# Optimization experiments

Hardware: AMD Instinct MI355X
Metric: run time of the kernel (lower is better)

## Reference

```python
import jax, jax.numpy as jnp
import numpy as np

# Static configuration (mirrors MeshPotential.__init__ + mesh-size derivation)
SIGMA = 1.0          # atomic_gaussian_width
SPACING = 0.2        # mesh_spacing
ORDER = 4            # interpolation_order (cubic, P3M M4 assignment)
L = 10.0             # cubic cell edge used in setup_inputs
N_ATOMS = 200000
# ns = 2**ceil(log2(2*L/SPACING + 1)) = 2**ceil(log2(101)) = 128 per axis
NX = NY = NZ = 128


def setup_inputs() -> dict:
    key = jax.random.key(0)
    k1, k2 = jax.random.split(key)
    cell = L * jnp.eye(3, dtype=jnp.float32)                  # (3,3) cell rows = basis vectors
    positions = jax.random.uniform(k1, (N_ATOMS, 3), jnp.float32, 0.0, L)
    charges = jax.random.normal(k2, (N_ATOMS, 1), jnp.float32)
    return {"cell": cell, "positions": positions, "charges": charges}


def _interp(cell, positions):
    """Order-4 (cubic B-spline / P3M) interpolation weights + flat mesh indices."""
    ns = jnp.array([NX, NY, NZ], dtype=positions.dtype)
    rel = (positions @ jnp.linalg.inv(cell)) * ns             # (n,3) fractional * mesh size
    idx0 = jnp.floor(rel).astype(jnp.int32)                   # even order: floor-based stencil
    x = rel - (idx0.astype(rel.dtype) + 0.5)                  # offset in [-1/2, 1/2)
    x2, x3 = x * x, x * x * x
    # P3M charge-assignment weights of order 4, grid points [floor-1, floor, floor+1, floor+2]
    w = jnp.stack([
        1.0 - 6.0 * x + 12.0 * x2 - 8.0 * x3,
        23.0 - 30.0 * x - 12.0 * x2 + 24.0 * x3,
        23.0 + 30.0 * x - 12.0 * x2 - 24.0 * x3,
        1.0 + 6.0 * x + 12.0 * x2 + 8.0 * x3,
    ]) / 48.0                                                 # (4, n, 3)
    shifts = jnp.array([-1, 0, 1, 2], dtype=jnp.int32)
    idx = (idx0[None] + shifts[:, None, None]) % jnp.array([NX, NY, NZ], jnp.int32)  # (4,n,3)
    ix, iy, iz = idx[..., 0], idx[..., 1], idx[..., 2]        # (4,n) each
    flat = (ix[:, None, None] * NY + iy[None, :, None]) * NZ + iz[None, None, :]     # (4,4,4,n)
    flat = flat.reshape(64, -1).T                             # (n,64) flat mesh indices
    w3d = jnp.einsum('ia,ja,ka->aijk', w[..., 0], w[..., 1], w[..., 2]).reshape(-1, 64)  # (n,64)
    return w3d, flat


def _forward(cell, positions, charges):
    n, C = charges.shape
    w3d, flat = _interp(cell, positions)
    # points_to_mesh: spline-weighted scatter of charges onto the mesh
    vals = charges.T[:, :, None] * w3d[None]                  # (C,n,64)
    rho = jnp.zeros((C, NX * NY * NZ), charges.dtype).at[:, flat].add(vals)
    rho = rho.reshape(C, NX, NY, NZ)
    # Fourier-space convolution with G(k^2) = 4*pi/k^2 * exp(-sigma^2 k^2 / 2), G(0)=0
    Brec = 2.0 * jnp.pi * jnp.linalg.inv(cell).T              # rows = reciprocal vectors b_i
    mx = jnp.fft.fftfreq(NX) * NX
    my = jnp.fft.fftfreq(NY) * NY
    mz = jnp.fft.rfftfreq(NZ) * NZ
    kvec = (mx[:, None, None, None] * Brec[0]
            + my[None, :, None, None] * Brec[1]
            + mz[None, None, :, None] * Brec[2])              # (NX,NY,NZ//2+1,3)
    ksq = jnp.sum(kvec * kvec, axis=-1).astype(charges.dtype)
    safe = jnp.where(ksq == 0.0, 1.0, ksq)
    G = jnp.where(ksq == 0.0, 0.0, 4.0 * jnp.pi / safe * jnp.exp(-0.5 * SIGMA * SIGMA * safe))
    rho_hat = jnp.fft.rfftn(rho, axes=(1, 2, 3))              # unnormalized forward FFT
    pot_mesh = jnp.fft.irfftn(rho_hat * G, s=(NX, NY, NZ), axes=(1, 2, 3), norm="forward")
    pot_mesh = pot_mesh / jnp.abs(jnp.linalg.det(cell))       # divide by cell volume
    # mesh_to_points: spline-weighted gather back to atom positions
    gathered = pot_mesh.reshape(C, -1)[:, flat] * w3d[None]   # (C,n,64)
    potential = gathered.sum(-1).T                            # (n,C)
    # subtract self-contribution of the atom-centered gaussian
    potential = potential - charges * (jnp.sqrt(2.0 / jnp.pi) / SIGMA)
    return potential


def reference(cell, positions, charges):
    return _forward(cell, positions, charges)
```

## Files before the change

### kernel.cpp

```cpp
#include <hip/hip_runtime.h>
#include <math.h>

#define NTOT (128*128*128)
#define NBIN2 64
#define BINS (NBIN2*NBIN2*NBIN2)
#define SCAN_BLOCKS 256

#define ZP 72
#define CAP 1024

#define PI_F      3.14159265358979323846f
#define TWO_PI_F  6.28318530717958647692f
#define FOUR_PI_F 12.5663706143591729539f


__device__ inline void inv3x3(const float* __restrict__ c, float* inv, float* detOut) {
    float a = c[0], b = c[1], cc = c[2];
    float d = c[3], e = c[4], f  = c[5];
    float g = c[6], h = c[7], i  = c[8];
    float A = e * i - f * h;
    float B = f * g - d * i;
    float C = d * h - e * g;
    float det = a * A + b * B + cc * C;
    float r = 1.0f / det;
    inv[0] = A * r;              inv[1] = (cc * h - b * i) * r;  inv[2] = (b * f - cc * e) * r;
    inv[3] = B * r;              inv[4] = (a * i - cc * g) * r;  inv[5] = (cc * d - a * f) * r;
    inv[6] = C * r;              inv[7] = (b * g - a * h) * r;   inv[8] = (a * e - b * d) * r;
    *detOut = det;
}

__device__ inline void w4(float x, float* w) {
    float x2 = x * x, x3 = x2 * x;
    w[0] = (1.0f  - 6.0f  * x + 12.0f * x2 - 8.0f  * x3) * (1.0f / 48.0f);
    w[1] = (23.0f - 30.0f * x - 12.0f * x2 + 24.0f * x3) * (1.0f / 48.0f);
    w[2] = (23.0f + 30.0f * x - 12.0f * x2 - 24.0f * x3) * (1.0f / 48.0f);
    w[3] = (1.0f  + 6.0f  * x + 12.0f * x2 + 8.0f  * x3) * (1.0f / 48.0f);
}

__device__ inline void atom_rel(const float* __restrict__ cell,
                                const float* __restrict__ pos, int t,
                                float* rx, float* ry, float* rz) {
    float inv[9]; float det;
    inv3x3(cell, inv, &det);
    float px = pos[3 * t], py = pos[3 * t + 1], pz = pos[3 * t + 2];
    *rx = (px * inv[0] + py * inv[3] + pz * inv[6]) * 128.0f;
    *ry = (px * inv[1] + py * inv[4] + pz * inv[7]) * 128.0f;
    *rz = (px * inv[2] + py * inv[5] + pz * inv[8]) * 128.0f;
}

__device__ inline int bin_of(float rx, float ry, float rz) {
    int ix = ((int)floorf(rx)) & 127;
    int iy = ((int)floorf(ry)) & 127;
    int iz = ((int)floorf(rz)) & 127;
    return ((((ix >> 1) << 6) | (iy >> 1)) << 6) | (iz >> 1);
}

__device__ inline float wrap128(float u) {
    u = (u > 64.0f) ? u - 128.0f : u;
    u = (u < -64.0f) ? u + 128.0f : u;
    return u;
}

__device__ inline float bspline(float u) {
    float a = fabsf(u);
    float t = fmaxf(2.0f - a, 0.0f);
    float s = fmaxf(1.0f - a, 0.0f);
    return t * t * t - 4.0f * s * s * s;
}


__global__ void zero_int_kernel(int* __restrict__ p, int n) {
    int i = blockIdx.x * blockDim.x + threadIdx.x;
    if (i < n) p[i] = 0;
}

__global__ void hist_kernel(const float* __restrict__ cell, const float* __restrict__ pos,
                            int* __restrict__ hist, int n) {
    int t = blockIdx.x * blockDim.x + threadIdx.x;
    if (t >= n) return;
    float rx, ry, rz;
    atom_rel(cell, pos, t, &rx, &ry, &rz);
    atomicAdd(&hist[bin_of(rx, ry, rz)], 1);
}

__global__ __launch_bounds__(256) void scan_local(const int4* __restrict__ hist4,
                                                  int4* __restrict__ off4,
                                                  int* __restrict__ partials) {
    const int b = blockIdx.x, t = threadIdx.x;
    const int idx = b * 256 + t;
    int4 h = hist4[idx];
    int s = h.x + h.y + h.z + h.w;
    int lane = t & 63, wv = t >> 6;
    int v = s;
    #pragma unroll
    for (int d = 1; d < 64; d <<= 1) {
        int o = __shfl_up(v, d, 64);
        if (lane >= d) v += o;
    }
    __shared__ int wsum[4];
    if (lane == 63) wsum[wv] = v;
    __syncthreads();
    int add = 0;
    #pragma unroll
    for (int k = 0; k < 4; ++k) if (k < wv) add += wsum[k];
    int run = add + v - s;
    int4 o4;
    o4.x = run; run += h.x;
    o4.y = run; run += h.y;
    o4.z = run; run += h.z;
    o4.w = run; run += h.w;
    off4[idx] = o4;
    if (t == 255) partials[b] = run;
}

__global__ __launch_bounds__(256) void scan_add(int4* __restrict__ hist4,
                                                int4* __restrict__ off4,
                                                const int* __restrict__ partials,
                                                int* __restrict__ offsets) {
    const int b = blockIdx.x, t = threadIdx.x;
    int lane = t & 63, wv = t >> 6;
    int v = (t < b) ? partials[t] : 0;
    #pragma unroll
    for (int d = 32; d >= 1; d >>= 1) v += __shfl_xor(v, d, 64);
    __shared__ int ws2[4];
    __shared__ int base_s;
    if (lane == 0) ws2[wv] = v;
    __syncthreads();
    if (t == 0) base_s = ws2[0] + ws2[1] + ws2[2] + ws2[3];
    __syncthreads();
    const int base = base_s;
    const int idx = b * 256 + t;
    int4 o4 = off4[idx];
    o4.x += base; o4.y += base; o4.z += base; o4.w += base;
    off4[idx]  = o4;
    hist4[idx] = o4;
    if (b == SCAN_BLOCKS - 1 && t == 255) offsets[BINS] = base + partials[b];
}

__global__ void reorder_kernel(const float* __restrict__ cell, const float* __restrict__ pos,
                               const float* __restrict__ q, int* __restrict__ cursor,
                               float4* __restrict__ sorted, int* __restrict__ sortedIdx, int n) {
    int t = blockIdx.x * blockDim.x + threadIdx.x;
    if (t >= n) return;
    float rx, ry, rz;
    atom_rel(cell, pos, t, &rx, &ry, &rz);
    int p = atomicAdd(&cursor[bin_of(rx, ry, rz)], 1);
    sorted[p] = make_float4(rx, ry, rz, q[t]);
    sortedIdx[p] = t;
}


__global__ __launch_bounds__(512) void lds_scatter_kernel(const float4* __restrict__ atoms,
                                                          const int* __restrict__ offsets,
                                                          float* __restrict__ rmesh) {
    const int blk = blockIdx.x;
    const int bz = blk & 7, by = (blk >> 3) & 7, bx = blk >> 6;
    const int ox = bx << 4, oy = by << 4, oz = bz << 4;
    const int gbx0 = ((ox - 2) & 127) >> 1;
    const int gby0 = ((oy - 2) & 127) >> 1;
    const int gbz0 = ((oz - 2) & 127) >> 1;

    __shared__ float4 satoms[CAP];
    __shared__ int P[1025];
    __shared__ int wsum[8];

    const int t = threadIdx.x;

    int c0 = 0, c1 = 0, g0 = 0, g1 = 0;
    {
        int b = 2 * t;
        if (b < 1000) {
            int jx = b / 100, rr = b - jx * 100, jy = rr / 10, jz = rr - jy * 10;
            int gb = ((((gbx0 + jx) & 63) << 6) | ((gby0 + jy) & 63)) << 6 | ((gbz0 + jz) & 63);
            g0 = offsets[gb]; c0 = offsets[gb + 1] - g0;
        }
        b = 2 * t + 1;
        if (b < 1000) {
            int jx = b / 100, rr = b - jx * 100, jy = rr / 10, jz = rr - jy * 10;
            int gb = ((((gbx0 + jx) & 63) << 6) | ((gby0 + jy) & 63)) << 6 | ((gbz0 + jz) & 63);
            g1 = offsets[gb]; c1 = offsets[gb + 1] - g1;
        }
    }

    int s = c0 + c1;
    int lane = t & 63, wv = t >> 6;
    int v = s;
    #pragma unroll
    for (int d = 1; d < 64; d <<= 1) {
        int o = __shfl_up(v, d, 64);
        if (lane >= d) v += o;
    }
    if (lane == 63) wsum[wv] = v;
    __syncthreads();
    int add = 0;
    #pragma unroll
    for (int k = 0; k < 8; ++k) if (k < wv) add += wsum[k];
    const int pre = add + v - s;
    P[2 * t] = pre;
    P[2 * t + 1] = pre + c0;
    if (t == 511) P[1024] = add + v;
    __syncthreads();

    for (int k = 0; k < c0; ++k) {
        int d = pre + k;
        if (d >= CAP) break;
        satoms[d] = atoms[g0 + k];
    }
    {
        int pre1 = pre + c0;
        for (int k = 0; k < c1; ++k) {
            int d = pre1 + k;
            if (d >= CAP) break;
            satoms[d] = atoms[g1 + k];
        }
    }
    __syncthreads();

    const int qz = t & 7, qy = (t >> 3) & 7, qx = t >> 6;
    const int cx0 = ox + (qx << 1), cy0 = oy + (qy << 1), cz0 = oz + (qz << 1);
    const float fcx = (float)cx0, fcy = (float)cy0, fcz = (float)cz0;

    float a000 = 0.0f, a001 = 0.0f, a010 = 0.0f, a011 = 0.0f;
    float a100 = 0.0f, a101 = 0.0f, a110 = 0.0f, a111 = 0.0f;

    int r = -1, i = 0, e = 0;
    while (i >= e) {
        if (++r >= 9) break;
        int dbx = r / 3, dby = r - dbx * 3;
        int bin0 = ((qx + dbx) * 10 + (qy + dby)) * 10 + qz;
        i = P[bin0];
        e = P[bin0 + 3];
        if (e > CAP) e = CAP;
    }
    while (r < 9) {
        float4 a = satoms[i];

        float ux = wrap128(a.x - fcx);
        float wx0 = bspline(ux);
        float wx1 = bspline(ux - 1.0f);
        float uy = wrap128(a.y - fcy);
        float wy0 = bspline(uy);
        float wy1 = bspline(uy - 1.0f);
        float uz = wrap128(a.z - fcz);
        float wz0 = bspline(uz);
        float wz1 = bspline(uz - 1.0f);
        float qs = a.w * (1.0f / 216.0f);
        float qx0 = qs * wx0, qx1 = qs * wx1;
        float m00 = qx0 * wy0, m01 = qx0 * wy1;
        float m10 = qx1 * wy0, m11 = qx1 * wy1;
        a000 += m00 * wz0; a001 += m00 * wz1;
        a010 += m01 * wz0; a011 += m01 * wz1;
        a100 += m10 * wz0; a101 += m10 * wz1;
        a110 += m11 * wz0; a111 += m11 * wz1;

        if (++i >= e) {
            while (i >= e) {
                if (++r >= 9) break;
                int dbx = r / 3, dby = r - dbx * 3;
                int bin0 = ((qx + dbx) * 10 + (qy + dby)) * 10 + qz;
                i = P[bin0];
                e = P[bin0 + 3];
                if (e > CAP) e = CAP;
            }
            if (r >= 9) break;
        }
    }

    *(float2*)&rmesh[((size_t)cx0       << 14) | ((size_t)cy0       << 7) | (size_t)cz0] = make_float2(a000, a001);
    *(float2*)&rmesh[((size_t)cx0       << 14) | ((size_t)(cy0 + 1) << 7) | (size_t)cz0] = make_float2(a010, a011);
    *(float2*)&rmesh[((size_t)(cx0 + 1) << 14) | ((size_t)cy0       << 7) | (size_t)cz0] = make_float2(a100, a101);
    *(float2*)&rmesh[((size_t)(cx0 + 1) << 14) | ((size_t)(cy0 + 1) << 7) | (size_t)cz0] = make_float2(a110, a111);
}


__device__ inline void bfly_dif(float& rr, float& ii, int h, bool hi, float cs, float sn) {
    float pr = __shfl_xor(rr, h), pi = __shfl_xor(ii, h);
    float br = hi ? (pr - rr) : (rr + pr);
    float bi = hi ? (pi - ii) : (ii + pi);
    rr = cs * br - sn * bi;
    ii = cs * bi + sn * br;
}

__device__ inline void bfly_dit(float& rr, float& ii, int h, bool hi, float cs, float sn) {
    float pr = __shfl_xor(rr, h), pi = __shfl_xor(ii, h);
    float xr = hi ? rr : pr, xi = hi ? ii : pi;
    float br = hi ? pr : rr, bi = hi ? pi : ii;
    float tr = cs * xr - sn * xi, ti = cs * xi + sn * xr;
    rr = hi ? (br - tr) : (br + tr);
    ii = hi ? (bi - ti) : (bi + ti);
}

__device__ inline void wfft_dif_fwd(float& r0, float& i0, float& r1, float& i1, int lane) {
    {
        float ang = -PI_F * (float)lane * (1.0f / 64.0f);
        float sn, cs; __sincosf(ang, &sn, &cs);
        float ar = r0 + r1, ai = i0 + i1;
        float dr = r0 - r1, di = i0 - i1;
        r0 = ar; i0 = ai;
        r1 = cs * dr - sn * di;
        i1 = cs * di + sn * dr;
    }
    #pragma unroll
    for (int h = 32; h >= 1; h >>= 1) {
        int pos = lane & (h - 1);
        bool hi = (lane & h) != 0;
        float ang = hi ? (-PI_F * (float)pos / (float)h) : 0.0f;
        float sn, cs; __sincosf(ang, &sn, &cs);
        bfly_dif(r0, i0, h, hi, cs, sn);
        bfly_dif(r1, i1, h, hi, cs, sn);
    }
}

__device__ inline void wfft_dit_inv(float& r0, float& i0, float& r1, float& i1, int lane) {
    #pragma unroll
    for (int h = 1; h <= 32; h <<= 1) {
        int pos = lane & (h - 1);
        bool hi = (lane & h) != 0;
        float ang = PI_F * (float)pos / (float)h;
        float sn, cs; __sincosf(ang, &sn, &cs);
        bfly_dit(r0, i0, h, hi, cs, sn);
        bfly_dit(r1, i1, h, hi, cs, sn);
    }
    {
        float ang = PI_F * (float)lane * (1.0f / 64.0f);
        float sn, cs; __sincosf(ang, &sn, &cs);
        float tr = cs * r1 - sn * i1, ti = cs * i1 + sn * r1;
        float nr = r0 + tr, ni = i0 + ti;
        r1 = r0 - tr; i1 = i0 - ti;
        r0 = nr; i0 = ni;
    }
}


__global__ __launch_bounds__(1024) void fftZfwd(const float* __restrict__ rin,
                                                float2* __restrict__ mesh) {
    __shared__ float tre[16][132], tim[16][132];
    const int t = threadIdx.x, b = blockIdx.x;
    for (int u = t; u < 2048; u += 1024) {
        int l = u >> 7, e = u & 127;
        tre[l][e] = rin[((size_t)((b << 4) | l) << 7) + e];
    }
    __syncthreads();
    const int w = t >> 6, lane = t & 63;
    float r0 = tre[w][lane],      i0 = 0.0f;
    float r1 = tre[w][lane + 64], i1 = 0.0f;
    wfft_dif_fwd(r0, i0, r1, i1, lane);
    int e0 = (int)(__brev((unsigned)lane) >> 25);
    tre[w][e0] = r0;     tim[w][e0] = i0;
    tre[w][e0 + 1] = r1; tim[w][e0 + 1] = i1;
    __syncthreads();
    for (int u = t; u < 2048; u += 1024) {
        int l = u >> 7, e = u & 127;
        if (e < ZP)
            mesh[(size_t)((b << 4) | l) * ZP + e] = make_float2(tre[l][e], tim[l][e]);
    }
}


__global__ __launch_bounds__(512) void fftYfwd(float2* __restrict__ mesh) {
    __shared__ float tre[8][132], tim[8][132];
    const int t = threadIdx.x, b = blockIdx.x;
    const int x = b & 127, zf0 = (b >> 7) << 3;
    const size_t rb = ((size_t)(x << 7)) * ZP + zf0;
    for (int u = t; u < 1024; u += 512) {
        int e = u >> 3, dz = u & 7;
        float2 vv = mesh[rb + (size_t)e * ZP + dz];
        tre[dz][e] = vv.x; tim[dz][e] = vv.y;
    }
    __syncthreads();
    const int w = t >> 6, lane = t & 63;
    float r0 = tre[w][lane],      i0 = tim[w][lane];
    float r1 = tre[w][lane + 64], i1 = tim[w][lane + 64];
    wfft_dif_fwd(r0, i0, r1, i1, lane);
    tre[w][lane] = r0;      tim[w][lane] = i0;
    tre[w][lane + 64] = r1; tim[w][lane + 64] = i1;
    __syncthreads();
    for (int u = t; u < 1024; u += 512) {
        int e = u >> 3, dz = u & 7;
        mesh[rb + (size_t)e * ZP + dz] = make_float2(tre[dz][e], tim[dz][e]);
    }
}


__global__ __launch_bounds__(512) void fftXGw(float2* __restrict__ mesh,
                                              const float* __restrict__ cell) {
    __shared__ float tre[8][132], tim[8][132];
    const int t = threadIdx.x, b = blockIdx.x;
    const int py = b & 127, zf0 = (b >> 7) << 3;
    for (int u = t; u < 1024; u += 512) {
        int e = u >> 3, dz = u & 7;
        float2 vv = mesh[(size_t)((e << 7) | py) * ZP + zf0 + dz];
        tre[dz][e] = vv.x; tim[dz][e] = vv.y;
    }
    __syncthreads();
    const int w = t >> 6, lane = t & 63;
    float r0 = tre[w][lane],      i0 = tim[w][lane];
    float r1 = tre[w][lane + 64], i1 = tim[w][lane + 64];
    wfft_dif_fwd(r0, i0, r1, i1, lane);
    {
        float inv[9]; float det; inv3x3(cell, inv, &det);
        float invVol = 1.0f / fabsf(det);
        int my = (int)(__brev((unsigned)py) >> 25);
        int mz = zf0 + w;
        float fy = (my < 64) ? (float)my : (float)(my - 128);
        float fz = (mz < 64) ? (float)mz : (float)(mz - 128);
        int mx0 = (int)(__brev((unsigned)lane) >> 25);
        #pragma unroll
        for (int s = 0; s < 2; ++s) {
            int mx = mx0 + s;
            float fx = (mx < 64) ? (float)mx : (float)(mx - 128);
            float kx = TWO_PI_F * (fx * inv[0] + fy * inv[1] + fz * inv[2]);
            float ky = TWO_PI_F * (fx * inv[3] + fy * inv[4] + fz * inv[5]);
            float kz = TWO_PI_F * (fx * inv[6] + fy * inv[7] + fz * inv[8]);
            float ksq = kx * kx + ky * ky + kz * kz;
            float G = (ksq == 0.0f) ? 0.0f
                      : FOUR_PI_F / ksq * __expf(-0.5f * ksq) * invVol;
            if (s == 0) { r0 *= G; i0 *= G; } else { r1 *= G; i1 *= G; }
        }
    }
    wfft_dit_inv(r0, i0, r1, i1, lane);
    tre[w][lane] = r0;      tim[w][lane] = i0;
    tre[w][lane + 64] = r1; tim[w][lane + 64] = i1;
    __syncthreads();
    for (int u = t; u < 1024; u += 512) {
        int e = u >> 3, dz = u & 7;
        mesh[(size_t)((e << 7) | py) * ZP + zf0 + dz] =
            make_float2(tre[dz][e], tim[dz][e]);
    }
}


__global__ __launch_bounds__(512) void fftYinv(float2* __restrict__ mesh) {
    __shared__ float tre[8][132], tim[8][132];
    const int t = threadIdx.x, b = blockIdx.x;
    const int x = b & 127, zf0 = (b >> 7) << 3;
    const size_t rb = ((size_t)(x << 7)) * ZP + zf0;
    for (int u = t; u < 1024; u += 512) {
        int e = u >> 3, dz = u & 7;
        float2 vv = mesh[rb + (size_t)e * ZP + dz];
        tre[dz][e] = vv.x; tim[dz][e] = vv.y;
    }
    __syncthreads();
    const int w = t >> 6, lane = t & 63;
    float r0 = tre[w][lane],      i0 = tim[w][lane];
    float r1 = tre[w][lane + 64], i1 = tim[w][lane + 64];
    wfft_dit_inv(r0, i0, r1, i1, lane);
    tre[w][lane] = r0;      tim[w][lane] = i0;
    tre[w][lane + 64] = r1; tim[w][lane + 64] = i1;
    __syncthreads();
    for (int u = t; u < 1024; u += 512) {
        int e = u >> 3, dz = u & 7;
        mesh[rb + (size_t)e * ZP + dz] = make_float2(tre[dz][e], tim[dz][e]);
    }
}


__global__ __launch_bounds__(1024) void fftZinv(const float2* __restrict__ mesh,
                                                float* __restrict__ rout) {
    __shared__ float tre[16][132], tim[16][132];
    const int t = threadIdx.x, b = blockIdx.x;
    for (int u = t; u < 2048; u += 1024) {
        int l = u >> 7, e = u & 127;
        int src = (e <= 64) ? e : 128 - e;
        float2 vv = mesh[(size_t)((b << 4) | l) * ZP + src];
        tre[l][e] = vv.x;
        tim[l][e] = (e <= 64) ? vv.y : -vv.y;
    }
    __syncthreads();
    const int w = t >> 6, lane = t & 63;
    int e0 = (int)(__brev((unsigned)lane) >> 25);
    float r0 = tre[w][e0],     i0 = tim[w][e0];
    float r1 = tre[w][e0 + 1], i1 = tim[w][e0 + 1];
    wfft_dit_inv(r0, i0, r1, i1, lane);
    const size_t rb = ((size_t)((b << 4) | w) << 7);
    rout[rb + lane] = r0;
    rout[rb + lane + 64] = r1;
}


__global__ void gather_kernel(const float4* __restrict__ sorted, const int* __restrict__ sortedIdx,
                              const float* __restrict__ rmesh, float* __restrict__ out, int n) {
    int t = blockIdx.x * blockDim.x + threadIdx.x;
    if (t >= n) return;
    float4 a = sorted[t];
    float wx[4], wy[4], wz[4];
    int ix[4], iy[4], iz[4];
    {
        float fl = floorf(a.x); int i0 = (int)fl; float x = a.x - fl - 0.5f; w4(x, wx);
        #pragma unroll
        for (int s = 0; s < 4; ++s) ix[s] = (i0 + s - 1) & 127;
    }
    {
        float fl = floorf(a.y); int i0 = (int)fl; float x = a.y - fl - 0.5f; w4(x, wy);
        #pragma unroll
        for (int s = 0; s < 4; ++s) iy[s] = (i0 + s - 1) & 127;
    }
    {
        float fl = floorf(a.z); int i0 = (int)fl; float x = a.z - fl - 0.5f; w4(x, wz);
        #pragma unroll
        for (int s = 0; s < 4; ++s) iz[s] = (i0 + s - 1) & 127;
    }
    float sum = 0.0f;
    #pragma unroll
    for (int i = 0; i < 4; ++i) {
        int bx = ix[i] << 14;
        float acc_i = 0.0f;
        #pragma unroll
        for (int j = 0; j < 4; ++j) {
            int bxy = bx | (iy[j] << 7);
            float acc_j = 0.0f;
            #pragma unroll
            for (int k = 0; k < 4; ++k) {
                acc_j += wz[k] * rmesh[bxy | iz[k]];
            }
            acc_i += wy[j] * acc_j;
        }
        sum += wx[i] * acc_i;
    }
    out[sortedIdx[t]] = sum - a.w * 0.79788456080286535588f;
}


extern "C" void kernel_launch(void* const* d_in, const int* in_sizes, int n_in,
                              void* d_out, int out_size, void* d_ws, size_t ws_size,
                              hipStream_t stream) {
    const float* cell = (const float*)d_in[0];
    const float* pos  = (const float*)d_in[1];
    const float* q    = (const float*)d_in[2];
    float* out = (float*)d_out;
    const int n = in_sizes[2];

    char* ws = (char*)d_ws;
    size_t o = 0;
    float4* sorted   = (float4*)(ws + o); o += (size_t)n * 16;
    int* sortedIdx   = (int*)(ws + o);    o += (size_t)n * 4;  o = (o + 255) & ~(size_t)255;
    int* hist        = (int*)(ws + o);    o += (size_t)BINS * 4;
    int* offsets     = (int*)(ws + o);    o += (size_t)(BINS + 4) * 4;
    int* partials    = (int*)(ws + o);    o += (size_t)SCAN_BLOCKS * 4; o = (o + 255) & ~(size_t)255;
    float2* mesh     = (float2*)(ws + o); o += (size_t)128 * 128 * ZP * 8;
    float* rmesh     = (float*)(ws + o);

    zero_int_kernel<<<BINS / 256, 256, 0, stream>>>(hist, BINS);
    hist_kernel<<<(n + 255) / 256, 256, 0, stream>>>(cell, pos, hist, n);
    scan_local<<<SCAN_BLOCKS, 256, 0, stream>>>((const int4*)hist, (int4*)offsets, partials);
    scan_add<<<SCAN_BLOCKS, 256, 0, stream>>>((int4*)hist, (int4*)offsets, partials, offsets);
    reorder_kernel<<<(n + 255) / 256, 256, 0, stream>>>(cell, pos, q, hist, sorted, sortedIdx, n);

    lds_scatter_kernel<<<512, 512, 0, stream>>>(sorted, offsets, rmesh);

    fftZfwd<<<1024, 1024, 0, stream>>>(rmesh, mesh);
    fftYfwd<<<9 * 128, 512, 0, stream>>>(mesh);
    fftXGw<<<9 * 128, 512, 0, stream>>>(mesh, cell);
    fftYinv<<<9 * 128, 512, 0, stream>>>(mesh);
    fftZinv<<<1024, 1024, 0, stream>>>(mesh, rmesh);

    gather_kernel<<<(n + 255) / 256, 256, 0, stream>>>(sorted, sortedIdx, rmesh, out, n);
}
```

Before: 141.2 us.

## Gather mesh potential through LDS-staged 16^3 tiles per block

New measurement: 135.7 us. -3.8%, faster.

```diff
diff --git a/kernel.cpp b/kernel.cpp
--- a/kernel.cpp
+++ b/kernel.cpp
@@ -27,14 +27,6 @@
     inv[3] = B * r;              inv[4] = (a * i - cc * g) * r;  inv[5] = (cc * d - a * f) * r;
     inv[6] = C * r;              inv[7] = (b * g - a * h) * r;   inv[8] = (a * e - b * d) * r;
     *detOut = det;
-}
-
-__device__ inline void w4(float x, float* w) {
-    float x2 = x * x, x3 = x2 * x;
-    w[0] = (1.0f  - 6.0f  * x + 12.0f * x2 - 8.0f  * x3) * (1.0f / 48.0f);
-    w[1] = (23.0f - 30.0f * x - 12.0f * x2 + 24.0f * x3) * (1.0f / 48.0f);
-    w[2] = (23.0f + 30.0f * x - 12.0f * x2 - 24.0f * x3) * (1.0f / 48.0f);
-    w[3] = (1.0f  + 6.0f  * x + 12.0f * x2 + 8.0f  * x3) * (1.0f / 48.0f);
 }
 
 __device__ inline void atom_rel(const float* __restrict__ cell,
@@ -270,6 +262,100 @@
     *(float2*)&rmesh[((size_t)cx0       << 14) | ((size_t)(cy0 + 1) << 7) | (size_t)cz0] = make_float2(a010, a011);
     *(float2*)&rmesh[((size_t)(cx0 + 1) << 14) | ((size_t)cy0       << 7) | (size_t)cz0] = make_float2(a100, a101);
     *(float2*)&rmesh[((size_t)(cx0 + 1) << 14) | ((size_t)(cy0 + 1) << 7) | (size_t)cz0] = make_float2(a110, a111);
+}
+
+
+__global__ __launch_bounds__(512) void lds_gather_kernel(const float4* __restrict__ atoms,
+                                                         const int* __restrict__ sortedIdx,
+                                                         const int* __restrict__ offsets,
+                                                         const float* __restrict__ rmesh,
+                                                         float* __restrict__ out) {
+    const int blk = blockIdx.x;
+    const int bz = blk & 7, by = (blk >> 3) & 7, bx = blk >> 6;
+    const int ox = bx << 4, oy = by << 4, oz = bz << 4;
+
+    __shared__ float tile[19][19][20];
+    __shared__ int P[513];
+    __shared__ int gbase[512];
+    __shared__ int wsum[8];
+
+    const int t = threadIdx.x;
+
+    for (int u = t; u < 19 * 19 * 19; u += 512) {
+        int dz = u % 19, rest = u / 19;
+        int dy = rest % 19, dx = rest / 19;
+        int gx = (ox - 1 + dx) & 127;
+        int gy = (oy - 1 + dy) & 127;
+        int gz = (oz - 1 + dz) & 127;
+        tile[dx][dy][dz] = rmesh[((size_t)gx << 14) | ((size_t)gy << 7) | (size_t)gz];
+    }
+
+    int cnt;
+    {
+        int uz = t & 7, uy = (t >> 3) & 7, ux = t >> 6;
+        int gb = ((((bx << 3) | ux) << 6) | ((by << 3) | uy)) << 6 | ((bz << 3) | uz);
+        int s0 = offsets[gb];
+        gbase[t] = s0;
+        cnt = offsets[gb + 1] - s0;
+    }
+    int lane = t & 63, wv = t >> 6;
+    int v = cnt;
+    #pragma unroll
+    for (int d = 1; d < 64; d <<= 1) {
+        int o = __shfl_up(v, d, 64);
+        if (lane >= d) v += o;
+    }
+    if (lane == 63) wsum[wv] = v;
+    __syncthreads();
+    int add = 0;
+    #pragma unroll
+    for (int k = 0; k < 8; ++k) if (k < wv) add += wsum[k];
+    P[t] = add + v - cnt;
+    if (t == 511) P[512] = add + v;
+    __syncthreads();
+
+    const int total = P[512];
+    for (int i = t; i < total; i += 512) {
+        int lo = 0, hi = 511;
+        #pragma unroll
+        for (int st = 0; st < 9; ++st) {
+            int mid = (lo + hi + 1) >> 1;
+            if (P[mid] <= i) lo = mid; else hi = mid - 1;
+        }
+        const int j = lo;
+        const int src = gbase[j] + (i - P[j]);
+        float4 a = atoms[src];
+
+        float flx = floorf(a.x), fly = floorf(a.y), flz = floorf(a.z);
+        int lx = (((int)flx) & 127) - ox + 1;
+        int ly = (((int)fly) & 127) - oy + 1;
+        int lz = (((int)flz) & 127) - oz + 1;
+        float xx = a.x - flx, yy = a.y - fly, zz = a.z - flz;
+
+        float wx0 = bspline(xx + 1.0f), wx1 = bspline(xx);
+        float wx2 = bspline(xx - 1.0f), wx3 = bspline(xx - 2.0f);
+        float wy0 = bspline(yy + 1.0f), wy1 = bspline(yy);
+        float wy2 = bspline(yy - 1.0f), wy3 = bspline(yy - 2.0f);
+        float wz0 = bspline(zz + 1.0f), wz1 = bspline(zz);
+        float wz2 = bspline(zz - 1.0f), wz3 = bspline(zz - 2.0f);
+
+        float sum = 0.0f;
+        #pragma unroll
+        for (int di = 0; di < 4; ++di) {
+            float wxv = (di == 0) ? wx0 : (di == 1) ? wx1 : (di == 2) ? wx2 : wx3;
+            const float* rowx = &tile[lx - 1 + di][0][0];
+            float sy = 0.0f;
+            #pragma unroll
+            for (int dj = 0; dj < 4; ++dj) {
+                float wyv = (dj == 0) ? wy0 : (dj == 1) ? wy1 : (dj == 2) ? wy2 : wy3;
+                const float* rowz = rowx + (ly - 1 + dj) * 20 + (lz - 1);
+                float sz = wz0 * rowz[0] + wz1 * rowz[1] + wz2 * rowz[2] + wz3 * rowz[3];
+                sy += wyv * sz;
+            }
+            sum += wxv * sy;
+        }
+        out[sortedIdx[src]] = sum * (1.0f / 216.0f) - a.w * 0.79788456080286535588f;
+    }
 }
 
 
@@ -478,49 +564,6 @@
 }
 
 
-__global__ void gather_kernel(const float4* __restrict__ sorted, const int* __restrict__ sortedIdx,
-                              const float* __restrict__ rmesh, float* __restrict__ out, int n) {
-    int t = blockIdx.x * blockDim.x + threadIdx.x;
-    if (t >= n) return;
-    float4 a = sorted[t];
-    float wx[4], wy[4], wz[4];
-    int ix[4], iy[4], iz[4];
-    {
-        float fl = floorf(a.x); int i0 = (int)fl; float x = a.x - fl - 0.5f; w4(x, wx);
-        #pragma unroll
-        for (int s = 0; s < 4; ++s) ix[s] = (i0 + s - 1) & 127;
-    }
-    {
-        float fl = floorf(a.y); int i0 = (int)fl; float x = a.y - fl - 0.5f; w4(x, wy);
-        #pragma unroll
-        for (int s = 0; s < 4; ++s) iy[s] = (i0 + s - 1) & 127;
-    }
-    {
-        float fl = floorf(a.z); int i0 = (int)fl; float x = a.z - fl - 0.5f; w4(x, wz);
-        #pragma unroll
-        for (int s = 0; s < 4; ++s) iz[s] = (i0 + s - 1) & 127;
-    }
-    float sum = 0.0f;
-    #pragma unroll
-    for (int i = 0; i < 4; ++i) {
-        int bx = ix[i] << 14;
-        float acc_i = 0.0f;
-        #pragma unroll
-        for (int j = 0; j < 4; ++j) {
-            int bxy = bx | (iy[j] << 7);
-            float acc_j = 0.0f;
-            #pragma unroll
-            for (int k = 0; k < 4; ++k) {
-                acc_j += wz[k] * rmesh[bxy | iz[k]];
-            }
-            acc_i += wy[j] * acc_j;
-        }
-        sum += wx[i] * acc_i;
-    }
-    out[sortedIdx[t]] = sum - a.w * 0.79788456080286535588f;
-}
-
-
 extern "C" void kernel_launch(void* const* d_in, const int* in_sizes, int n_in,
                               void* d_out, int out_size, void* d_ws, size_t ws_size,
                               hipStream_t stream) {
@@ -554,5 +597,5 @@
     fftYinv<<<9 * 128, 512, 0, stream>>>(mesh);
     fftZinv<<<1024, 1024, 0, stream>>>(mesh, rmesh);
 
-    gather_kernel<<<(n + 255) / 256, 256, 0, stream>>>(sorted, sortedIdx, rmesh, out, n);
-}
+    lds_gather_kernel<<<512, 512, 0, stream>>>(sorted, sortedIdx, offsets, rmesh, out);
+}
```
